# Performance work log

Hardware: AMD Instinct MI355X
Metric: run time of the kernel (lower is better)

## Reference

```python
import jax, jax.numpy as jnp
import numpy as np

N_NODES = 100000
M_NODES = 100000
N_EDGES = 1600000
D_IN = 128
HIDDEN = 128
D_OUT = 128


def setup_inputs() -> dict:
    key = jax.random.key(0)
    ks = jax.random.split(key, 10)
    s = 1.0 / np.sqrt(D_IN)
    return {
        "query": jax.random.normal(ks[0], (N_NODES, D_IN), dtype=jnp.float32),
        "memory": jax.random.normal(ks[1], (M_NODES, D_IN), dtype=jnp.float32),
        "Wq": jax.random.normal(ks[2], (D_IN, HIDDEN), dtype=jnp.float32) * s,
        "bq": jnp.zeros((HIDDEN,), dtype=jnp.float32),
        "Wk": jax.random.normal(ks[3], (D_IN, HIDDEN), dtype=jnp.float32) * s,
        "bk": jnp.zeros((HIDDEN,), dtype=jnp.float32),
        "Wv": jax.random.normal(ks[4], (D_IN, D_OUT), dtype=jnp.float32) * s,
        "bv": jnp.zeros((D_OUT,), dtype=jnp.float32),
        "edge_rows": jax.random.randint(ks[5], (N_EDGES,), 0, N_NODES, dtype=jnp.int32),
        "edge_cols": jax.random.randint(ks[6], (N_EDGES,), 0, M_NODES, dtype=jnp.int32),
    }


def reference(query, memory, Wq, bq, Wk, bk, Wv, bv, edge_rows, edge_cols):
    # Dense projections with gelu (tfa.activations.gelu ~ tanh-approx gelu)
    q = jax.nn.gelu(query @ Wq + bq)      # [n, hidden]
    k = jax.nn.gelu(memory @ Wk + bk)     # [m, hidden]
    v = jax.nn.gelu(memory @ Wv + bv)     # [m, d_out]
    scale = 1.0 / jnp.sqrt(jnp.asarray(HIDDEN, dtype=q.dtype))
    # Edge-wise gather-dot-sigmoid (matmul_with_sparse_mask)
    dot = jnp.sum(q[edge_rows] * k[edge_cols], axis=-1)  # [E]
    coef = jax.nn.sigmoid(dot * scale)                   # [E]
    # Sparse-dense matmul: aggregate v over edges into rows
    out = jax.ops.segment_sum(coef[:, None] * v[edge_cols], edge_rows,
                              num_segments=query.shape[0])  # [n, d_out]
    return out
```

## Files before the change

### kernel.cpp

```cpp
#include <hip/hip_runtime.h>
#include <hip/hip_bf16.h>
#include <math.h>

#ifndef __has_builtin
#define __has_builtin(x) 0
#endif
#if __has_builtin(__builtin_amdgcn_cvt_pk_fp8_f32) && __has_builtin(__builtin_amdgcn_cvt_pk_f32_fp8)
#define FP8_HW 1
#else
#include <hip/hip_fp8.h>
#endif

#define D 128
#define KVREC 384

typedef float f32x16 __attribute__((ext_vector_type(16)));
typedef float f32x2  __attribute__((ext_vector_type(2)));
typedef short bf16x8 __attribute__((ext_vector_type(8)));

__device__ __forceinline__ float gelu_fast(float x) {
    float u = 0.7978845608028654f * (x + 0.044715f * x * x * x);
    return x / (1.0f + __expf(-2.0f * u));
}

__device__ __forceinline__ unsigned short f2bf(float f) {
    union { float f; unsigned u; } x; x.f = f;
    unsigned r = x.u + 0x7fff + ((x.u >> 16) & 1);
    return (unsigned short)(r >> 16);
}

__device__ __forceinline__ float bflo(unsigned u) { return __uint_as_float(u << 16); }
__device__ __forceinline__ float bfhi(unsigned u) { return __uint_as_float(u & 0xffff0000u); }

__device__ __forceinline__ unsigned char f2fp8(float x) {
#ifdef FP8_HW
    return (unsigned char)(__builtin_amdgcn_cvt_pk_fp8_f32(x, x, 0, false) & 0xFF);
#else
    __hip_fp8_e4m3 h(x); return (unsigned char)h.__x;
#endif
}

__device__ __forceinline__ void fp8x4d(unsigned u, float* f) {
#ifdef FP8_HW
    f32x2 lo = __builtin_amdgcn_cvt_pk_f32_fp8((int)u, false);
    f32x2 hi = __builtin_amdgcn_cvt_pk_f32_fp8((int)u, true);
    f[0] = lo[0]; f[1] = lo[1]; f[2] = hi[0]; f[3] = hi[1];
#else
    #pragma unroll
    for (int i = 0; i < 4; ++i) {
        __hip_fp8_e4m3 h; h.__x = (unsigned char)((u >> (8 * i)) & 0xFF);
        f[i] = (float)h;
    }
#endif
}


__global__ __launch_bounds__(256) void fused_pre_kernel(
    const int* __restrict__ rows, int* __restrict__ cnt, int* __restrict__ rank,
    int nE, int n, int nbE8,
    const float* __restrict__ W0, const float* __restrict__ W1,
    const float* __restrict__ W2, unsigned short* __restrict__ F)
{
    const int bid = blockIdx.x;
    if (bid < nbE8) {
        const int g  = bid & 7;
        const int lo = (int)(((long long)g * n) >> 3);
        const int hi = (int)(((long long)(g + 1) * n) >> 3);
        const int idx = (bid >> 3) * 1024 + threadIdx.x * 4;
        if (idx + 3 < nE) {
            int4 r4 = *reinterpret_cast<const int4*>(rows + idx);
            int rk[4] = {-1, -1, -1, -1};
            if (r4.x >= lo && r4.x < hi) rk[0] = atomicAdd(&cnt[r4.x], 1);
            if (r4.y >= lo && r4.y < hi) rk[1] = atomicAdd(&cnt[r4.y], 1);
            if (r4.z >= lo && r4.z < hi) rk[2] = atomicAdd(&cnt[r4.z], 1);
            if (r4.w >= lo && r4.w < hi) rk[3] = atomicAdd(&cnt[r4.w], 1);
            #pragma unroll
            for (int j = 0; j < 4; ++j)
                if (rk[j] >= 0) rank[idx + j] = rk[j];
        } else {
            for (int i = 0; i < 4; ++i)
                if (idx + i < nE) {
                    int r = rows[idx + i];
                    if (r >= lo && r < hi) rank[idx + i] = atomicAdd(&cnt[r], 1);
                }
        }
    } else {
        int gidx = (bid - nbE8) * 256 + threadIdx.x;
        if (gidx >= 3 * 32 * 64 * 8) return;
        const int midx = gidx >> 14;
        const int idx  = gidx & 16383;
        const float* W = midx == 0 ? W0 : (midx == 1 ? W1 : W2);
        int j  = idx & 7;
        int l  = (idx >> 3) & 63;
        int kt = (idx >> 9) & 7;
        int ct = idx >> 12;
        int kk = kt * 16 + (l >> 5) * 8 + j;
        int c  = ct * 32 + (l & 31);
        F[gidx] = f2bf(W[kk * D + c]);
    }
}


__global__ __launch_bounds__(256) void scan_bsum_kernel(
    const int* __restrict__ cnt, int* __restrict__ bsum, int n)
{
    __shared__ int s[256];
    const int t = threadIdx.x;
    const int base = blockIdx.x * 1024 + t * 4;
    int sum = 0;
    if (base + 3 < n) {
        int4 c4 = *reinterpret_cast<const int4*>(cnt + base);
        sum = c4.x + c4.y + c4.z + c4.w;
    } else {
        for (int i = 0; i < 4; ++i) if (base + i < n) sum += cnt[base + i];
    }
    s[t] = sum;
    __syncthreads();
    #pragma unroll
    for (int off = 128; off > 0; off >>= 1) {
        if (t < off) s[t] += s[t + off];
        __syncthreads();
    }
    if (t == 0) bsum[blockIdx.x] = s[0];
}

__global__ __launch_bounds__(256) void scan_write2_kernel(
    const int* __restrict__ cnt, const int* __restrict__ bsum, int nb,
    int* __restrict__ rowptr, int n)
{
    __shared__ int s[256];
    const int t = threadIdx.x;

    s[t] = (t < nb) ? bsum[t] : 0;
    __syncthreads();
    #pragma unroll
    for (int off = 1; off < 256; off <<= 1) {
        int v = (t >= off) ? s[t - off] : 0;
        __syncthreads();
        s[t] += v;
        __syncthreads();
    }
    const int boffv = (blockIdx.x > 0) ? s[blockIdx.x - 1] : 0;
    const int total = s[255];
    if (blockIdx.x == 0 && t == 0) rowptr[n] = total;
    __syncthreads();

    const int base = blockIdx.x * 1024 + t * 4;
    int c[4] = {0, 0, 0, 0};
    if (base + 3 < n) {
        int4 c4 = *reinterpret_cast<const int4*>(cnt + base);
        c[0] = c4.x; c[1] = c4.y; c[2] = c4.z; c[3] = c4.w;
    } else {
        for (int i = 0; i < 4; ++i) if (base + i < n) c[i] = cnt[base + i];
    }
    const int tsum = c[0] + c[1] + c[2] + c[3];
    s[t] = tsum;
    __syncthreads();
    #pragma unroll
    for (int off = 1; off < 256; off <<= 1) {
        int v = (t >= off) ? s[t - off] : 0;
        __syncthreads();
        s[t] += v;
        __syncthreads();
    }
    int run = boffv + s[t] - tsum;
    int w0 = run;
    int w1 = run + c[0];
    int w2 = w1 + c[1];
    int w3 = w2 + c[2];
    if (base + 3 < n) {
        *reinterpret_cast<int4*>(rowptr + base) = make_int4(w0, w1, w2, w3);
    } else {
        int w[4] = {w0, w1, w2, w3};
        for (int i = 0; i < 4; ++i) if (base + i < n) rowptr[base + i] = w[i];
    }
}


__global__ __launch_bounds__(256, 8) void scatter_kernel(
    const int* __restrict__ rows, const int* __restrict__ cols,
    const int* __restrict__ rank, const int* __restrict__ rowptr,
    int* __restrict__ colsorted, int nE, int n)
{
    const int g  = blockIdx.x & 7;
    const int lo = (int)(((long long)g * n) >> 3);
    const int hi = (int)(((long long)(g + 1) * n) >> 3);
    const int idx = (blockIdx.x >> 3) * 2048 + threadIdx.x * 8;
    if (idx + 7 < nE) {
        int4 ra = *reinterpret_cast<const int4*>(rows + idx);
        int4 rb = *reinterpret_cast<const int4*>(rows + idx + 4);
        int4 ca = *reinterpret_cast<const int4*>(cols + idx);
        int4 cb = *reinterpret_cast<const int4*>(cols + idx + 4);
        int4 ka = *reinterpret_cast<const int4*>(rank + idx);
        int4 kb = *reinterpret_cast<const int4*>(rank + idx + 4);
        int r[8] = {ra.x, ra.y, ra.z, ra.w, rb.x, rb.y, rb.z, rb.w};
        int c[8] = {ca.x, ca.y, ca.z, ca.w, cb.x, cb.y, cb.z, cb.w};
        int k[8] = {ka.x, ka.y, ka.z, ka.w, kb.x, kb.y, kb.z, kb.w};
        int p[8];
        #pragma unroll
        for (int j = 0; j < 8; ++j)
            p[j] = (r[j] >= lo && r[j] < hi) ? rowptr[r[j]] + k[j] : -1;
        #pragma unroll
        for (int j = 0; j < 8; ++j)
            if (p[j] >= 0) colsorted[p[j]] = c[j];
    } else {
        for (int i = 0; i < 8; ++i)
            if (idx + i < nE) {
                int r = rows[idx + i];
                if (r >= lo && r < hi)
                    colsorted[rowptr[r] + rank[idx + i]] = cols[idx + i];
            }
    }
}


__global__ __launch_bounds__(256) void proj_kernel(
    const float* __restrict__ Xq, const float* __restrict__ Xm,
    const unsigned short* __restrict__ Fq, const float* __restrict__ bq,
    unsigned short* __restrict__ qout,
    const unsigned short* __restrict__ Fk, const float* __restrict__ bk,
    const unsigned short* __restrict__ Fv, const float* __restrict__ bv,
    unsigned char* __restrict__ kv,
    int n, int m, int nbQ)
{
    __shared__ __align__(16) unsigned short sX[64][136];
    const int bid = blockIdx.x;
    const int tid = threadIdx.x;

    const bool isQ = bid < nbQ;
    const int row0 = (isQ ? bid : bid - nbQ) * 64;
    const int nn   = isQ ? n : m;
    const float* X = isQ ? Xq : Xm;

    #pragma unroll
    for (int p = 0; p < 8; ++p) {
        int flat = p * 256 + tid;
        int r = flat >> 5;
        int c = (flat & 31) * 4;
        int gr = row0 + r; if (gr >= nn) gr = nn - 1;
        float4 x4 = *reinterpret_cast<const float4*>(X + (size_t)gr * D + c);
        uint2 pk;
        pk.x = (unsigned)f2bf(x4.x) | ((unsigned)f2bf(x4.y) << 16);
        pk.y = (unsigned)f2bf(x4.z) | ((unsigned)f2bf(x4.w) << 16);
        *reinterpret_cast<uint2*>(&sX[r][c]) = pk;
    }
    __syncthreads();

    const int l   = tid & 63;
    const int w   = tid >> 6;
    const int rg  = w >> 1;
    const int ct0 = (w & 1) * 2;
    const int arow = rg * 32 + (l & 31);
    const int rowbase = row0 + rg * 32;

    bf16x8 af[8];
    #pragma unroll
    for (int kt = 0; kt < 8; ++kt)
        af[kt] = *reinterpret_cast<const bf16x8*>(&sX[arow][kt * 16 + (l >> 5) * 8]);

    if (isQ) {
        #pragma unroll 1
        for (int ci = 0; ci < 2; ++ci) {
            const int ct = ct0 + ci;
            f32x16 acc = {};
            #pragma unroll
            for (int kt = 0; kt < 8; ++kt) {
                bf16x8 bfr = *reinterpret_cast<const bf16x8*>(Fq + ((size_t)((ct * 8 + kt) * 64 + l) * 8));
                acc = __builtin_amdgcn_mfma_f32_32x32x16_bf16(af[kt], bfr, acc, 0, 0, 0);
            }
            const int col = ct * 32 + (l & 31);
            const float bb = bq[col];
            #pragma unroll
            for (int reg = 0; reg < 16; ++reg) {
                int r  = (reg & 3) + 8 * (reg >> 2) + 4 * (l >> 5);
                int gr = rowbase + r;
                if (gr < nn)
                    qout[(size_t)gr * D + col] = f2bf(gelu_fast(acc[reg] + bb));
            }
        }
    } else {
        #pragma unroll 1
        for (int mat = 0; mat < 2; ++mat) {
            const unsigned short* F = mat ? Fv : Fk;
            const float* bias       = mat ? bv : bk;
            #pragma unroll 1
            for (int ci = 0; ci < 2; ++ci) {
                const int ct = ct0 + ci;
                f32x16 acc = {};
                #pragma unroll
                for (int kt = 0; kt < 8; ++kt) {
                    bf16x8 bfr = *reinterpret_cast<const bf16x8*>(F + ((size_t)((ct * 8 + kt) * 64 + l) * 8));
                    acc = __builtin_amdgcn_mfma_f32_32x32x16_bf16(af[kt], bfr, acc, 0, 0, 0);
                }
                const int col = ct * 32 + (l & 31);
                const float bb = bias[col];
                #pragma unroll
                for (int reg = 0; reg < 16; ++reg) {
                    int r  = (reg & 3) + 8 * (reg >> 2) + 4 * (l >> 5);
                    int gr = rowbase + r;
                    if (gr < nn) {
                        unsigned char* rec = kv + (size_t)gr * KVREC;
                        float val = gelu_fast(acc[reg] + bb);
                        if (mat == 0)
                            rec[col] = f2fp8(val);
                        else
                            reinterpret_cast<unsigned short*>(rec + 128)[col] = f2bf(val);
                    }
                }
            }
        }
    }
}

__global__ __launch_bounds__(256) void agg_kernel(
    const unsigned short* __restrict__ q, const unsigned char* __restrict__ kv,
    const int* __restrict__ rowptr, const int* __restrict__ colsorted,
    float* __restrict__ out, int n)
{
    const int wave = (blockIdx.x * 256 + threadIdx.x) >> 6;
    if (wave >= n) return;
    const int lane = threadIdx.x & 63;
    const int sub  = lane >> 4;
    const int l    = lane & 15;

    const uint4 qa = *reinterpret_cast<const uint4*>(q + (size_t)wave * D + l * 8);
    float qf[8];
    qf[0] = bflo(qa.x); qf[1] = bfhi(qa.x);
    qf[2] = bflo(qa.y); qf[3] = bfhi(qa.y);
    qf[4] = bflo(qa.z); qf[5] = bfhi(qa.z);
    qf[6] = bflo(qa.w); qf[7] = bfhi(qa.w);

    float acc[8] = {0.f,0.f,0.f,0.f,0.f,0.f,0.f,0.f};
    const int start = rowptr[wave], end = rowptr[wave + 1];

    #pragma unroll 2
    for (int i = start + sub; i < end; i += 4) {
        const int c = colsorted[i];
        const unsigned char* rec = kv + (size_t)c * KVREC;
        const uint2 kb = *reinterpret_cast<const uint2*>(rec + l * 8);
        const uint4 vb = *reinterpret_cast<const uint4*>(rec + 128 + l * 16);

        float kf[8];
        fp8x4d(kb.x, kf); fp8x4d(kb.y, kf + 4);

        float dot = 0.0f;
        #pragma unroll
        for (int j = 0; j < 8; ++j) dot = fmaf(qf[j], kf[j], dot);
        dot += __shfl_xor(dot, 1);
        dot += __shfl_xor(dot, 2);
        dot += __shfl_xor(dot, 4);
        dot += __shfl_xor(dot, 8);
        const float coef = 1.0f / (1.0f + __expf(-dot * 0.08838834764831845f));

        acc[0] = fmaf(coef, bflo(vb.x), acc[0]);
        acc[1] = fmaf(coef, bfhi(vb.x), acc[1]);
        acc[2] = fmaf(coef, bflo(vb.y), acc[2]);
        acc[3] = fmaf(coef, bfhi(vb.y), acc[3]);
        acc[4] = fmaf(coef, bflo(vb.z), acc[4]);
        acc[5] = fmaf(coef, bfhi(vb.z), acc[5]);
        acc[6] = fmaf(coef, bflo(vb.w), acc[6]);
        acc[7] = fmaf(coef, bfhi(vb.w), acc[7]);
    }

    #pragma unroll
    for (int j = 0; j < 8; ++j) {
        acc[j] += __shfl_xor(acc[j], 16);
        acc[j] += __shfl_xor(acc[j], 32);
    }

    if (sub == 0) {
        float* op = out + (size_t)wave * D + l * 8;
        float4 o0 = {acc[0], acc[1], acc[2], acc[3]};
        float4 o1 = {acc[4], acc[5], acc[6], acc[7]};
        *reinterpret_cast<float4*>(op)     = o0;
        *reinterpret_cast<float4*>(op + 4) = o1;
    }
}

extern "C" void kernel_launch(void* const* d_in, const int* in_sizes, int n_in,
                              void* d_out, int out_size, void* d_ws, size_t ws_size,
                              hipStream_t stream) {
    const float* query  = (const float*)d_in[0];
    const float* memory = (const float*)d_in[1];
    const float* Wq     = (const float*)d_in[2];
    const float* bq     = (const float*)d_in[3];
    const float* Wk     = (const float*)d_in[4];
    const float* bk     = (const float*)d_in[5];
    const float* Wv     = (const float*)d_in[6];
    const float* bv     = (const float*)d_in[7];
    const int*   erows  = (const int*)d_in[8];
    const int*   ecols  = (const int*)d_in[9];

    const int n  = in_sizes[0] / D;
    const int m  = in_sizes[1] / D;
    const int nE = in_sizes[8];

    char* base = (char*)d_ws;
    size_t off = 0;
    auto carve = [&](size_t bytes) -> char* {
        char* p = base + off;
        off = (off + bytes + 255) & ~(size_t)255;
        return p;
    };
    unsigned short* q   = (unsigned short*)carve((size_t)n * D * sizeof(unsigned short));
    unsigned char*  kv  = (unsigned char*) carve((size_t)m * KVREC);
    unsigned short* F   = (unsigned short*)carve(3 * 32 * 64 * 8 * sizeof(unsigned short));
    int*   rowptr    = (int*)carve((size_t)(n + 1) * sizeof(int));
    int*   cnt       = (int*)carve((size_t)(n + 1) * sizeof(int));
    int*   rank      = (int*)carve((size_t)nE * sizeof(int));
    int*   bsum      = (int*)carve(256 * sizeof(int));
    int*   colsorted = (int*)carve((size_t)nE * sizeof(int));
    float* out       = (float*)d_out;

    unsigned short* Fq = F;
    unsigned short* Fk = F + 16384;
    unsigned short* Fv = F + 32768;

    dim3 blk(256);
    const int nbScan = (n + 1023) / 1024;
    const int nbE8   = ((nE + 1023) / 1024) * 8;
    const int nbSc   = ((nE + 2047) / 2048) * 8;
    const int nbQ    = (n + 63) / 64;
    const int nbM    = (m + 63) / 64;

    hipMemsetAsync(cnt, 0, (size_t)(n + 1) * sizeof(int), stream);
    fused_pre_kernel<<<dim3(nbE8 + 192), blk, 0, stream>>>(
        erows, cnt, rank, nE, n, nbE8, Wq, Wk, Wv, F);
    scan_bsum_kernel<<<dim3(nbScan), blk, 0, stream>>>(cnt, bsum, n);
    scan_write2_kernel<<<dim3(nbScan), blk, 0, stream>>>(cnt, bsum, nbScan, rowptr, n);
    scatter_kernel<<<dim3(nbSc), blk, 0, stream>>>(erows, ecols, rank, rowptr, colsorted, nE, n);
    proj_kernel<<<dim3(nbQ + nbM), blk, 0, stream>>>(
        query, memory, Fq, bq, q, Fk, bk, Fv, bv, kv, n, m, nbQ);
    agg_kernel<<<dim3((n * 64 + 255) / 256), blk, 0, stream>>>(q, kv, rowptr, colsorted, out, n);
}
```

Measured before the change: 286.0 us.

## Split projection into persistent double-buffered Q and KV kernels; halve scatter row groups

Replaces the single proj_kernel with separate Q and KV kernels that use a fixed 1024-block persistent grid over 32-row tiles. Each kernel prefetches the next tile's fp32 rows into registers while the MFMA work runs on the current tile, using double-buffered LDS. The aim is to hide global load latency and cut block launch overhead. The scatter kernel also drops from 8 to 4 row partitions, which halves the redundant passes over the edge arrays at the cost of less write locality per pass.

```diff
diff --git a/kernel.cpp b/kernel.cpp
--- a/kernel.cpp
+++ b/kernel.cpp
@@ -182,10 +182,10 @@
     const int* __restrict__ rank, const int* __restrict__ rowptr,
     int* __restrict__ colsorted, int nE, int n)
 {
-    const int g  = blockIdx.x & 7;
-    const int lo = (int)(((long long)g * n) >> 3);
-    const int hi = (int)(((long long)(g + 1) * n) >> 3);
-    const int idx = (blockIdx.x >> 3) * 2048 + threadIdx.x * 8;
+    const int g  = blockIdx.x & 3;
+    const int lo = (int)(((long long)g * n) >> 2);
+    const int hi = (int)(((long long)(g + 1) * n) >> 2);
+    const int idx = (blockIdx.x >> 2) * 2048 + threadIdx.x * 8;
     if (idx + 7 < nE) {
         int4 ra = *reinterpret_cast<const int4*>(rows + idx);
         int4 rb = *reinterpret_cast<const int4*>(rows + idx + 4);
@@ -214,101 +214,165 @@
 }
 
 
-__global__ __launch_bounds__(256) void proj_kernel(
-    const float* __restrict__ Xq, const float* __restrict__ Xm,
-    const unsigned short* __restrict__ Fq, const float* __restrict__ bq,
-    unsigned short* __restrict__ qout,
+__global__ __launch_bounds__(256) void proj_q_kernel(
+    const float* __restrict__ X, const unsigned short* __restrict__ F1,
+    const float* __restrict__ b1, unsigned short* __restrict__ C1,
+    int n, int nTiles)
+{
+    __shared__ __align__(16) unsigned short sX[2][32][136];
+    const int tid = threadIdx.x;
+    const int l = tid & 63;
+    const int ct = tid >> 6;
+    const int arow = l & 31;
+
+    int tile = blockIdx.x;
+    if (tile >= nTiles) return;
+
+    float4 r4[4];
+    auto LOAD = [&](int t) {
+        const int row0 = t * 32;
+        #pragma unroll
+        for (int p = 0; p < 4; ++p) {
+            int flat = p * 256 + tid;
+            int rr = flat >> 5;
+            int cc = (flat & 31) * 4;
+            int gr = row0 + rr; if (gr >= n) gr = n - 1;
+            r4[p] = *reinterpret_cast<const float4*>(X + (size_t)gr * D + cc);
+        }
+    };
+    auto STORE_LDS = [&](int buf) {
+        #pragma unroll
+        for (int p = 0; p < 4; ++p) {
+            int flat = p * 256 + tid;
+            int rr = flat >> 5;
+            int cc = (flat & 31) * 4;
+            uint2 pk;
+            pk.x = (unsigned)f2bf(r4[p].x) | ((unsigned)f2bf(r4[p].y) << 16);
+            pk.y = (unsigned)f2bf(r4[p].z) | ((unsigned)f2bf(r4[p].w) << 16);
+            *reinterpret_cast<uint2*>(&sX[buf][rr][cc]) = pk;
+        }
+    };
+
+    LOAD(tile);
+    STORE_LDS(0);
+    int cur = 0;
+    const float bb = b1[ct * 32 + (l & 31)];
+    while (tile < nTiles) {
+        const int next = tile + gridDim.x;
+        __syncthreads();
+        if (next < nTiles) LOAD(next);
+
+        const int row0 = tile * 32;
+        bf16x8 af[8];
+        #pragma unroll
+        for (int kt = 0; kt < 8; ++kt)
+            af[kt] = *reinterpret_cast<const bf16x8*>(&sX[cur][arow][kt * 16 + (l >> 5) * 8]);
+        f32x16 acc = {};
+        #pragma unroll
+        for (int kt = 0; kt < 8; ++kt) {
+            bf16x8 bfr = *reinterpret_cast<const bf16x8*>(F1 + ((size_t)((ct * 8 + kt) * 64 + l) * 8));
+            acc = __builtin_amdgcn_mfma_f32_32x32x16_bf16(af[kt], bfr, acc, 0, 0, 0);
+        }
+        const int col = ct * 32 + (l & 31);
+        #pragma unroll
+        for (int reg = 0; reg < 16; ++reg) {
+            int rr = (reg & 3) + 8 * (reg >> 2) + 4 * (l >> 5);
+            int gr = row0 + rr;
+            if (gr < n)
+                C1[(size_t)gr * D + col] = f2bf(gelu_fast(acc[reg] + bb));
+        }
+
+        if (next < nTiles) STORE_LDS(cur ^ 1);
+        cur ^= 1;
+        tile = next;
+    }
+}
+
+__global__ __launch_bounds__(256) void proj_kv_kernel(
+    const float* __restrict__ X,
     const unsigned short* __restrict__ Fk, const float* __restrict__ bk,
     const unsigned short* __restrict__ Fv, const float* __restrict__ bv,
-    unsigned char* __restrict__ kv,
-    int n, int m, int nbQ)
-{
-    __shared__ __align__(16) unsigned short sX[64][136];
-    const int bid = blockIdx.x;
+    unsigned char* __restrict__ kv, int m, int nTiles)
+{
+    __shared__ __align__(16) unsigned short sX[2][32][136];
     const int tid = threadIdx.x;
-
-    const bool isQ = bid < nbQ;
-    const int row0 = (isQ ? bid : bid - nbQ) * 64;
-    const int nn   = isQ ? n : m;
-    const float* X = isQ ? Xq : Xm;
-
-    #pragma unroll
-    for (int p = 0; p < 8; ++p) {
-        int flat = p * 256 + tid;
-        int r = flat >> 5;
-        int c = (flat & 31) * 4;
-        int gr = row0 + r; if (gr >= nn) gr = nn - 1;
-        float4 x4 = *reinterpret_cast<const float4*>(X + (size_t)gr * D + c);
-        uint2 pk;
-        pk.x = (unsigned)f2bf(x4.x) | ((unsigned)f2bf(x4.y) << 16);
-        pk.y = (unsigned)f2bf(x4.z) | ((unsigned)f2bf(x4.w) << 16);
-        *reinterpret_cast<uint2*>(&sX[r][c]) = pk;
-    }
-    __syncthreads();
-
-    const int l   = tid & 63;
-    const int w   = tid >> 6;
-    const int rg  = w >> 1;
-    const int ct0 = (w & 1) * 2;
-    const int arow = rg * 32 + (l & 31);
-    const int rowbase = row0 + rg * 32;
-
-    bf16x8 af[8];
-    #pragma unroll
-    for (int kt = 0; kt < 8; ++kt)
-        af[kt] = *reinterpret_cast<const bf16x8*>(&sX[arow][kt * 16 + (l >> 5) * 8]);
-
-    if (isQ) {
+    const int l = tid & 63;
+    const int ct = tid >> 6;
+    const int arow = l & 31;
+
+    int tile = blockIdx.x;
+    if (tile >= nTiles) return;
+
+    float4 r4[4];
+    auto LOAD = [&](int t) {
+        const int row0 = t * 32;
+        #pragma unroll
+        for (int p = 0; p < 4; ++p) {
+            int flat = p * 256 + tid;
+            int rr = flat >> 5;
+            int cc = (flat & 31) * 4;
+            int gr = row0 + rr; if (gr >= m) gr = m - 1;
+            r4[p] = *reinterpret_cast<const float4*>(X + (size_t)gr * D + cc);
+        }
+    };
+    auto STORE_LDS = [&](int buf) {
+        #pragma unroll
+        for (int p = 0; p < 4; ++p) {
+            int flat = p * 256 + tid;
+            int rr = flat >> 5;
+            int cc = (flat & 31) * 4;
+            uint2 pk;
+            pk.x = (unsigned)f2bf(r4[p].x) | ((unsigned)f2bf(r4[p].y) << 16);
+            pk.y = (unsigned)f2bf(r4[p].z) | ((unsigned)f2bf(r4[p].w) << 16);
+            *reinterpret_cast<uint2*>(&sX[buf][rr][cc]) = pk;
+        }
+    };
+
+    LOAD(tile);
+    STORE_LDS(0);
+    int cur = 0;
+    const int col = ct * 32 + (l & 31);
+    const float bbk = bk[col];
+    const float bbv = bv[col];
+    while (tile < nTiles) {
+        const int next = tile + gridDim.x;
+        __syncthreads();
+        if (next < nTiles) LOAD(next);
+
+        const int row0 = tile * 32;
+        bf16x8 af[8];
+        #pragma unroll
+        for (int kt = 0; kt < 8; ++kt)
+            af[kt] = *reinterpret_cast<const bf16x8*>(&sX[cur][arow][kt * 16 + (l >> 5) * 8]);
+
         #pragma unroll 1
-        for (int ci = 0; ci < 2; ++ci) {
-            const int ct = ct0 + ci;
+        for (int mat = 0; mat < 2; ++mat) {
+            const unsigned short* F = mat ? Fv : Fk;
+            const float bb          = mat ? bbv : bbk;
             f32x16 acc = {};
             #pragma unroll
             for (int kt = 0; kt < 8; ++kt) {
-                bf16x8 bfr = *reinterpret_cast<const bf16x8*>(Fq + ((size_t)((ct * 8 + kt) * 64 + l) * 8));
+                bf16x8 bfr = *reinterpret_cast<const bf16x8*>(F + ((size_t)((ct * 8 + kt) * 64 + l) * 8));
                 acc = __builtin_amdgcn_mfma_f32_32x32x16_bf16(af[kt], bfr, acc, 0, 0, 0);
             }
-            const int col = ct * 32 + (l & 31);
-            const float bb = bq[col];
             #pragma unroll
             for (int reg = 0; reg < 16; ++reg) {
-                int r  = (reg & 3) + 8 * (reg >> 2) + 4 * (l >> 5);
-                int gr = rowbase + r;
-                if (gr < nn)
-                    qout[(size_t)gr * D + col] = f2bf(gelu_fast(acc[reg] + bb));
-            }
-        }
-    } else {
-        #pragma unroll 1
-        for (int mat = 0; mat < 2; ++mat) {
-            const unsigned short* F = mat ? Fv : Fk;
-            const float* bias       = mat ? bv : bk;
-            #pragma unroll 1
-            for (int ci = 0; ci < 2; ++ci) {
-                const int ct = ct0 + ci;
-                f32x16 acc = {};
-                #pragma unroll
-                for (int kt = 0; kt < 8; ++kt) {
-                    bf16x8 bfr = *reinterpret_cast<const bf16x8*>(F + ((size_t)((ct * 8 + kt) * 64 + l) * 8));
-                    acc = __builtin_amdgcn_mfma_f32_32x32x16_bf16(af[kt], bfr, acc, 0, 0, 0);
-                }
-                const int col = ct * 32 + (l & 31);
-                const float bb = bias[col];
-                #pragma unroll
-                for (int reg = 0; reg < 16; ++reg) {
-                    int r  = (reg & 3) + 8 * (reg >> 2) + 4 * (l >> 5);
-                    int gr = rowbase + r;
-                    if (gr < nn) {
-                        unsigned char* rec = kv + (size_t)gr * KVREC;
-                        float val = gelu_fast(acc[reg] + bb);
-                        if (mat == 0)
-                            rec[col] = f2fp8(val);
-                        else
-                            reinterpret_cast<unsigned short*>(rec + 128)[col] = f2bf(val);
-                    }
+                int rr = (reg & 3) + 8 * (reg >> 2) + 4 * (l >> 5);
+                int gr = row0 + rr;
+                if (gr < m) {
+                    unsigned char* rec = kv + (size_t)gr * KVREC;
+                    float val = gelu_fast(acc[reg] + bb);
+                    if (mat == 0)
+                        rec[col] = f2fp8(val);
+                    else
+                        reinterpret_cast<unsigned short*>(rec + 128)[col] = f2bf(val);
                 }
             }
         }
+
+        if (next < nTiles) STORE_LDS(cur ^ 1);
+        cur ^= 1;
+        tile = next;
     }
 }
 
@@ -419,9 +483,9 @@
     dim3 blk(256);
     const int nbScan = (n + 1023) / 1024;
     const int nbE8   = ((nE + 1023) / 1024) * 8;
-    const int nbSc   = ((nE + 2047) / 2048) * 8;
-    const int nbQ    = (n + 63) / 64;
-    const int nbM    = (m + 63) / 64;
+    const int nbSc   = ((nE + 2047) / 2048) * 4;
+    const int nTq    = (n + 31) / 32;
+    const int nTm    = (m + 31) / 32;
 
     hipMemsetAsync(cnt, 0, (size_t)(n + 1) * sizeof(int), stream);
     fused_pre_kernel<<<dim3(nbE8 + 192), blk, 0, stream>>>(
@@ -429,7 +493,7 @@
     scan_bsum_kernel<<<dim3(nbScan), blk, 0, stream>>>(cnt, bsum, n);
     scan_write2_kernel<<<dim3(nbScan), blk, 0, stream>>>(cnt, bsum, nbScan, rowptr, n);
     scatter_kernel<<<dim3(nbSc), blk, 0, stream>>>(erows, ecols, rank, rowptr, colsorted, nE, n);
-    proj_kernel<<<dim3(nbQ + nbM), blk, 0, stream>>>(
-        query, memory, Fq, bq, q, Fk, bk, Fv, bv, kv, n, m, nbQ);
+    proj_q_kernel<<<dim3(1024), blk, 0, stream>>>(query, Fq, bq, q, n, nTq);
+    proj_kv_kernel<<<dim3(1024), blk, 0, stream>>>(memory, Fk, bk, Fv, bv, kv, m, nTm);
     agg_kernel<<<dim3((n * 64 + 255) / 256), blk, 0, stream>>>(q, kv, rowptr, colsorted, out, n);
 }
```

Result: faster. 271.8 us (-5.0%).

## Fuse scatter and projection into one launch with persistent double-buffered tiles

Applied to the files above, without the earlier changes.

Merges the CSR scatter kernel and the projection GEMM kernel into a single launch, so the scatter blocks and the projection blocks can run at the same time. The projection becomes persistent: a fixed grid of 1024 blocks per side walks 32-row tiles, with register prefetch and a double-buffered LDS stage to overlap global loads with MFMA work. The scatter row-partitioning drops from 8 to 4 groups, and the aggregation loop prefetches column indices two iterations ahead. The risks are lower occupancy or poorer load balance in the persistent loop, and more scatter write traffic per block.

```diff
diff --git a/kernel.cpp b/kernel.cpp
--- a/kernel.cpp
+++ b/kernel.cpp
@@ -177,127 +177,138 @@
 }
 
 
-__global__ __launch_bounds__(256, 8) void scatter_kernel(
+__global__ __launch_bounds__(256) void fused_mid_kernel(
     const int* __restrict__ rows, const int* __restrict__ cols,
     const int* __restrict__ rank, const int* __restrict__ rowptr,
-    int* __restrict__ colsorted, int nE, int n)
-{
-    const int g  = blockIdx.x & 7;
-    const int lo = (int)(((long long)g * n) >> 3);
-    const int hi = (int)(((long long)(g + 1) * n) >> 3);
-    const int idx = (blockIdx.x >> 3) * 2048 + threadIdx.x * 8;
-    if (idx + 7 < nE) {
-        int4 ra = *reinterpret_cast<const int4*>(rows + idx);
-        int4 rb = *reinterpret_cast<const int4*>(rows + idx + 4);
-        int4 ca = *reinterpret_cast<const int4*>(cols + idx);
-        int4 cb = *reinterpret_cast<const int4*>(cols + idx + 4);
-        int4 ka = *reinterpret_cast<const int4*>(rank + idx);
-        int4 kb = *reinterpret_cast<const int4*>(rank + idx + 4);
-        int r[8] = {ra.x, ra.y, ra.z, ra.w, rb.x, rb.y, rb.z, rb.w};
-        int c[8] = {ca.x, ca.y, ca.z, ca.w, cb.x, cb.y, cb.z, cb.w};
-        int k[8] = {ka.x, ka.y, ka.z, ka.w, kb.x, kb.y, kb.z, kb.w};
-        int p[8];
-        #pragma unroll
-        for (int j = 0; j < 8; ++j)
-            p[j] = (r[j] >= lo && r[j] < hi) ? rowptr[r[j]] + k[j] : -1;
-        #pragma unroll
-        for (int j = 0; j < 8; ++j)
-            if (p[j] >= 0) colsorted[p[j]] = c[j];
-    } else {
-        for (int i = 0; i < 8; ++i)
-            if (idx + i < nE) {
-                int r = rows[idx + i];
-                if (r >= lo && r < hi)
-                    colsorted[rowptr[r] + rank[idx + i]] = cols[idx + i];
-            }
-    }
-}
-
-
-__global__ __launch_bounds__(256) void proj_kernel(
+    int* __restrict__ colsorted, int nE, int n, int nbSc,
     const float* __restrict__ Xq, const float* __restrict__ Xm,
     const unsigned short* __restrict__ Fq, const float* __restrict__ bq,
     unsigned short* __restrict__ qout,
     const unsigned short* __restrict__ Fk, const float* __restrict__ bk,
     const unsigned short* __restrict__ Fv, const float* __restrict__ bv,
-    unsigned char* __restrict__ kv,
-    int n, int m, int nbQ)
+    unsigned char* __restrict__ kv, int m, int nTq, int nTm, int nbP)
 {
-    __shared__ __align__(16) unsigned short sX[64][136];
+    __shared__ __align__(16) unsigned short sX[2][32][136];
     const int bid = blockIdx.x;
     const int tid = threadIdx.x;
 
-    const bool isQ = bid < nbQ;
-    const int row0 = (isQ ? bid : bid - nbQ) * 64;
+    if (bid < nbSc) {
+        const int g  = bid & 3;
+        const int lo = (int)(((long long)g * n) >> 2);
+        const int hi = (int)(((long long)(g + 1) * n) >> 2);
+        const int idx = (bid >> 2) * 2048 + tid * 8;
+        if (idx + 7 < nE) {
+            int4 ra = *reinterpret_cast<const int4*>(rows + idx);
+            int4 rb = *reinterpret_cast<const int4*>(rows + idx + 4);
+            int4 ca = *reinterpret_cast<const int4*>(cols + idx);
+            int4 cb = *reinterpret_cast<const int4*>(cols + idx + 4);
+            int4 ka = *reinterpret_cast<const int4*>(rank + idx);
+            int4 kb = *reinterpret_cast<const int4*>(rank + idx + 4);
+            int r[8] = {ra.x, ra.y, ra.z, ra.w, rb.x, rb.y, rb.z, rb.w};
+            int c[8] = {ca.x, ca.y, ca.z, ca.w, cb.x, cb.y, cb.z, cb.w};
+            int k[8] = {ka.x, ka.y, ka.z, ka.w, kb.x, kb.y, kb.z, kb.w};
+            int p[8];
+            #pragma unroll
+            for (int j = 0; j < 8; ++j)
+                p[j] = (r[j] >= lo && r[j] < hi) ? rowptr[r[j]] + k[j] : -1;
+            #pragma unroll
+            for (int j = 0; j < 8; ++j)
+                if (p[j] >= 0) colsorted[p[j]] = c[j];
+        } else {
+            for (int i = 0; i < 8; ++i)
+                if (idx + i < nE) {
+                    int r = rows[idx + i];
+                    if (r >= lo && r < hi)
+                        colsorted[rowptr[r] + rank[idx + i]] = cols[idx + i];
+                }
+        }
+        return;
+    }
+
+    const int pb  = bid - nbSc;
+    const bool isQ = pb < nbP;
+    const float* X = isQ ? Xq : Xm;
     const int nn   = isQ ? n : m;
-    const float* X = isQ ? Xq : Xm;
-
-    #pragma unroll
-    for (int p = 0; p < 8; ++p) {
-        int flat = p * 256 + tid;
-        int r = flat >> 5;
-        int c = (flat & 31) * 4;
-        int gr = row0 + r; if (gr >= nn) gr = nn - 1;
-        float4 x4 = *reinterpret_cast<const float4*>(X + (size_t)gr * D + c);
-        uint2 pk;
-        pk.x = (unsigned)f2bf(x4.x) | ((unsigned)f2bf(x4.y) << 16);
-        pk.y = (unsigned)f2bf(x4.z) | ((unsigned)f2bf(x4.w) << 16);
-        *reinterpret_cast<uint2*>(&sX[r][c]) = pk;
-    }
-    __syncthreads();
-
-    const int l   = tid & 63;
-    const int w   = tid >> 6;
-    const int rg  = w >> 1;
-    const int ct0 = (w & 1) * 2;
-    const int arow = rg * 32 + (l & 31);
-    const int rowbase = row0 + rg * 32;
-
-    bf16x8 af[8];
-    #pragma unroll
-    for (int kt = 0; kt < 8; ++kt)
-        af[kt] = *reinterpret_cast<const bf16x8*>(&sX[arow][kt * 16 + (l >> 5) * 8]);
-
-    if (isQ) {
-        #pragma unroll 1
-        for (int ci = 0; ci < 2; ++ci) {
-            const int ct = ct0 + ci;
+    const int nT   = isQ ? nTq : nTm;
+    int tile       = isQ ? pb : pb - nbP;
+    if (tile >= nT) return;
+
+    const int l = tid & 63;
+    const int ct = tid >> 6;
+    const int arow = l & 31;
+    const int col = ct * 32 + (l & 31);
+
+    float4 r4[4];
+    auto LOAD = [&](int t) {
+        const int row0 = t * 32;
+        #pragma unroll
+        for (int p = 0; p < 4; ++p) {
+            int flat = p * 256 + tid;
+            int rr = flat >> 5;
+            int cc = (flat & 31) * 4;
+            int gr = row0 + rr; if (gr >= nn) gr = nn - 1;
+            r4[p] = *reinterpret_cast<const float4*>(X + (size_t)gr * D + cc);
+        }
+    };
+    auto STORE_LDS = [&](int buf) {
+        #pragma unroll
+        for (int p = 0; p < 4; ++p) {
+            int flat = p * 256 + tid;
+            int rr = flat >> 5;
+            int cc = (flat & 31) * 4;
+            uint2 pk;
+            pk.x = (unsigned)f2bf(r4[p].x) | ((unsigned)f2bf(r4[p].y) << 16);
+            pk.y = (unsigned)f2bf(r4[p].z) | ((unsigned)f2bf(r4[p].w) << 16);
+            *reinterpret_cast<uint2*>(&sX[buf][rr][cc]) = pk;
+        }
+    };
+
+    LOAD(tile);
+    STORE_LDS(0);
+    int cur = 0;
+    const float bb1 = isQ ? bq[col] : bk[col];
+    const float bb2 = isQ ? 0.0f : bv[col];
+
+    while (tile < nT) {
+        const int next = tile + nbP;
+        __syncthreads();
+        if (next < nT) LOAD(next);
+
+        const int row0 = tile * 32;
+        bf16x8 af[8];
+        #pragma unroll
+        for (int kt = 0; kt < 8; ++kt)
+            af[kt] = *reinterpret_cast<const bf16x8*>(&sX[cur][arow][kt * 16 + (l >> 5) * 8]);
+
+        if (isQ) {
             f32x16 acc = {};
             #pragma unroll
             for (int kt = 0; kt < 8; ++kt) {
                 bf16x8 bfr = *reinterpret_cast<const bf16x8*>(Fq + ((size_t)((ct * 8 + kt) * 64 + l) * 8));
                 acc = __builtin_amdgcn_mfma_f32_32x32x16_bf16(af[kt], bfr, acc, 0, 0, 0);
             }
-            const int col = ct * 32 + (l & 31);
-            const float bb = bq[col];
             #pragma unroll
             for (int reg = 0; reg < 16; ++reg) {
-                int r  = (reg & 3) + 8 * (reg >> 2) + 4 * (l >> 5);
-                int gr = rowbase + r;
+                int rr = (reg & 3) + 8 * (reg >> 2) + 4 * (l >> 5);
+                int gr = row0 + rr;
                 if (gr < nn)
-                    qout[(size_t)gr * D + col] = f2bf(gelu_fast(acc[reg] + bb));
+                    qout[(size_t)gr * D + col] = f2bf(gelu_fast(acc[reg] + bb1));
             }
-        }
-    } else {
-        #pragma unroll 1
-        for (int mat = 0; mat < 2; ++mat) {
-            const unsigned short* F = mat ? Fv : Fk;
-            const float* bias       = mat ? bv : bk;
+        } else {
             #pragma unroll 1
-            for (int ci = 0; ci < 2; ++ci) {
-                const int ct = ct0 + ci;
+            for (int mat = 0; mat < 2; ++mat) {
+                const unsigned short* F = mat ? Fv : Fk;
+                const float bb          = mat ? bb2 : bb1;
                 f32x16 acc = {};
                 #pragma unroll
                 for (int kt = 0; kt < 8; ++kt) {
                     bf16x8 bfr = *reinterpret_cast<const bf16x8*>(F + ((size_t)((ct * 8 + kt) * 64 + l) * 8));
                     acc = __builtin_amdgcn_mfma_f32_32x32x16_bf16(af[kt], bfr, acc, 0, 0, 0);
                 }
-                const int col = ct * 32 + (l & 31);
-                const float bb = bias[col];
                 #pragma unroll
                 for (int reg = 0; reg < 16; ++reg) {
-                    int r  = (reg & 3) + 8 * (reg >> 2) + 4 * (l >> 5);
-                    int gr = rowbase + r;
+                    int rr = (reg & 3) + 8 * (reg >> 2) + 4 * (l >> 5);
+                    int gr = row0 + rr;
                     if (gr < nn) {
                         unsigned char* rec = kv + (size_t)gr * KVREC;
                         float val = gelu_fast(acc[reg] + bb);
@@ -309,6 +320,10 @@
                 }
             }
         }
+
+        if (next < nT) STORE_LDS(cur ^ 1);
+        cur ^= 1;
+        tile = next;
     }
 }
 
@@ -333,9 +348,16 @@
     float acc[8] = {0.f,0.f,0.f,0.f,0.f,0.f,0.f,0.f};
     const int start = rowptr[wave], end = rowptr[wave + 1];
 
+    int i  = start + sub;
+    int cA = (i     < end) ? colsorted[i]     : 0;
+    int cB = (i + 4 < end) ? colsorted[i + 4] : 0;
+
     #pragma unroll 2
-    for (int i = start + sub; i < end; i += 4) {
-        const int c = colsorted[i];
+    for (; i < end; i += 4) {
+        const int c = cA;
+        cA = cB;
+        cB = (i + 8 < end) ? colsorted[i + 8] : 0;
+
         const unsigned char* rec = kv + (size_t)c * KVREC;
         const uint2 kb = *reinterpret_cast<const uint2*>(rec + l * 8);
         const uint4 vb = *reinterpret_cast<const uint4*>(rec + 128 + l * 16);
@@ -419,17 +441,18 @@
     dim3 blk(256);
     const int nbScan = (n + 1023) / 1024;
     const int nbE8   = ((nE + 1023) / 1024) * 8;
-    const int nbSc   = ((nE + 2047) / 2048) * 8;
-    const int nbQ    = (n + 63) / 64;
-    const int nbM    = (m + 63) / 64;
+    const int nbSc   = ((nE + 2047) / 2048) * 4;
+    const int nTq    = (n + 31) / 32;
+    const int nTm    = (m + 31) / 32;
+    const int nbP    = 1024;
 
     hipMemsetAsync(cnt, 0, (size_t)(n + 1) * sizeof(int), stream);
     fused_pre_kernel<<<dim3(nbE8 + 192), blk, 0, stream>>>(
         erows, cnt, rank, nE, n, nbE8, Wq, Wk, Wv, F);
     scan_bsum_kernel<<<dim3(nbScan), blk, 0, stream>>>(cnt, bsum, n);
     scan_write2_kernel<<<dim3(nbScan), blk, 0, stream>>>(cnt, bsum, nbScan, rowptr, n);
-    scatter_kernel<<<dim3(nbSc), blk, 0, stream>>>(erows, ecols, rank, rowptr, colsorted, nE, n);
-    proj_kernel<<<dim3(nbQ + nbM), blk, 0, stream>>>(
-        query, memory, Fq, bq, q, Fk, bk, Fv, bv, kv, n, m, nbQ);
+    fused_mid_kernel<<<dim3(nbSc + 2 * nbP), blk, 0, stream>>>(
+        erows, ecols, rank, rowptr, colsorted, nE, n, nbSc,
+        query, memory, Fq, bq, q, Fk, bk, Fv, bv, kv, m, nTq, nTm, nbP);
     agg_kernel<<<dim3((n * 64 + 255) / 256), blk, 0, stream>>>(q, kv, rowptr, colsorted, out, n);
 }
```

After: 259.5 us. 1.1x faster.
